# Optimization experiments

Measured on AMD Instinct MI355X. Metric: run time of the kernel, lower is better.

## Reference

```python
import jax, jax.numpy as jnp
import numpy as np
from jax.ops import segment_sum, segment_max

N = 50000
E = 800000
F_IN = 128
F_HEAD = 32
HEADS = 8
N_CLASSES = 32
NEG_SLOPE = 0.2


def setup_inputs() -> dict:
    key = jax.random.key(0)
    ks = jax.random.split(key, 12)
    x = jax.random.normal(ks[0], (N, F_IN), dtype=jnp.float32)
    edge_index = jax.random.randint(ks[1], (2, E), 0, N, dtype=jnp.int64)
    # layer 1 params (in=128 -> heads=8, out=32)
    s1 = 1.0 / np.sqrt(F_IN)
    W1 = jax.random.uniform(ks[2], (F_IN, HEADS * F_HEAD), jnp.float32, -s1, s1)
    a_src1 = jax.random.uniform(ks[3], (HEADS, F_HEAD), jnp.float32, -s1, s1)
    a_dst1 = jax.random.uniform(ks[4], (HEADS, F_HEAD), jnp.float32, -s1, s1)
    b1 = jnp.zeros((HEADS * F_HEAD,), jnp.float32)
    # layer 2 params (in=256 -> heads=1, out=32)
    s2 = 1.0 / np.sqrt(HEADS * F_HEAD)
    W2 = jax.random.uniform(ks[5], (HEADS * F_HEAD, N_CLASSES), jnp.float32, -s2, s2)
    a_src2 = jax.random.uniform(ks[6], (1, N_CLASSES), jnp.float32, -s2, s2)
    a_dst2 = jax.random.uniform(ks[7], (1, N_CLASSES), jnp.float32, -s2, s2)
    b2 = jnp.zeros((N_CLASSES,), jnp.float32)
    return {"x": x, "edge_index": edge_index, "W1": W1, "a_src1": a_src1,
            "a_dst1": a_dst1, "b1": b1, "W2": W2, "a_src2": a_src2,
            "a_dst2": a_dst2, "b2": b2}


def gat_conv(x, W, a_src, a_dst, b, src, dst, heads, out_ch):
    n = x.shape[0]
    h = (x @ W).reshape(n, heads, out_ch)                  # [N,H,F]
    alpha_src = jnp.einsum('nhf,hf->nh', h, a_src)         # [N,H]
    alpha_dst = jnp.einsum('nhf,hf->nh', h, a_dst)
    e = alpha_src[src] + alpha_dst[dst]                    # [E,H]
    e = jnp.where(e > 0, e, NEG_SLOPE * e)                 # LeakyReLU(0.2)
    # segment softmax over edges grouped by destination node
    m = segment_max(e, dst, num_segments=n)                # [N,H]
    ex = jnp.exp(e - m[dst])
    denom = segment_sum(ex, dst, num_segments=n)           # [N,H]
    alpha = ex / (denom[dst] + 1e-16)                      # [E,H]
    out = segment_sum(alpha[:, :, None] * h[src], dst, num_segments=n)  # [N,H,F]
    return out.reshape(n, heads * out_ch) + b


def reference(x, edge_index, W1, a_src1, a_dst1, b1, W2, a_src2, a_dst2, b2):
    src, dst = edge_index[0], edge_index[1]
    h = gat_conv(x, W1, a_src1, a_dst1, b1, src, dst, HEADS, F_HEAD)
    h = jax.nn.elu(h)
    out = gat_conv(h, W2, a_src2, a_dst2, b2, src, dst, 1, N_CLASSES)
    return out
```

## Files before the change

### kernel.cpp

```cpp
#include <hip/hip_runtime.h>
#include <math.h>

#define NNODES 50000
#define NEDGES 800000
#define GB 782

typedef _Float16 f16;
typedef _Float16 f16x8 __attribute__((ext_vector_type(8)));
typedef _Float16 f16x4 __attribute__((ext_vector_type(4)));
typedef _Float16 f16x2 __attribute__((ext_vector_type(2)));
typedef float f32x4 __attribute__((ext_vector_type(4)));
typedef float f32x8 __attribute__((ext_vector_type(8)));


__global__ __launch_bounds__(256) void k_deg_wfrag(const int* __restrict__ ei, int* __restrict__ deg,
                                                   int* __restrict__ rank,
                                                   const float* __restrict__ W1, const float* __restrict__ W2,
                                                   f16* __restrict__ W1f, f16* __restrict__ W2f) {
    int bid = blockIdx.x;
    if (bid < NEDGES / 256) {
        int e = bid * 256 + threadIdx.x;
        rank[e] = atomicAdd(&deg[ei[NEDGES + e]], 1);
    } else {
        int id = (bid - NEDGES / 256) * 256 + threadIdx.x;
        if (id < 32768) {
            int k = id >> 8, c = id & 255;
            int kc = k >> 5, quad = (k & 31) >> 3, j = k & 7;
            W1f[(((kc << 8) + c) * 4 + quad) * 8 + j] = (f16)W1[id];
        } else {
            int i2 = id - 32768;
            int k = i2 >> 5, c = i2 & 31;
            int kc = k >> 5, quad = (k & 31) >> 3, j = k & 7;
            W2f[(((kc << 5) + c) * 4 + quad) * 8 + j] = (f16)W2[i2];
        }
    }
}

__global__ __launch_bounds__(256) void k_scanA(const int* __restrict__ deg, int* __restrict__ incl,
                                               int* __restrict__ partial) {
    int t = threadIdx.x;
    int i = blockIdx.x * 256 + t;
    int v = (i < NNODES) ? deg[i] : 0;
    int lane = t & 63, wid = t >> 6;
    int s = v;
#pragma unroll
    for (int d = 1; d < 64; d <<= 1) { int u = __shfl_up(s, d, 64); if (lane >= d) s += u; }
    __shared__ int wtot[4];
    if (lane == 63) wtot[wid] = s;
    __syncthreads();
    int off = 0;
    for (int w = 0; w < wid; ++w) off += wtot[w];
    s += off;
    if (i < NNODES) incl[i] = s;
    if (t == 255) partial[blockIdx.x] = s;
}

__global__ __launch_bounds__(256) void k_scanC(const int* __restrict__ deg, const int* __restrict__ incl,
                                               const int* __restrict__ partial, int* __restrict__ rowst) {
    int t = threadIdx.x, bid = blockIdx.x;
    int v = (t < bid) ? partial[t] : 0;
    int lane = t & 63, wid = t >> 6;
#pragma unroll
    for (int d = 1; d < 64; d <<= 1) v += __shfl_xor(v, d);
    __shared__ int ws[4];
    if (lane == 0) ws[wid] = v;
    __syncthreads();
    int choff = ws[0] + ws[1] + ws[2] + ws[3];
    int i = bid * 256 + t;
    if (i < NNODES) {
        int rs1 = incl[i] + choff;
        rowst[i + 1] = rs1;
        if (i == 0) rowst[0] = 0;
    }
}


__global__ __launch_bounds__(256) void k_gemm1_sc(const float* __restrict__ X, const f16* __restrict__ W1f,
                                                  const float* __restrict__ Asrc, const float* __restrict__ Adst,
                                                  f16* __restrict__ h1h, float* __restrict__ as1,
                                                  float* __restrict__ ad1, const int* __restrict__ ei,
                                                  const int* __restrict__ rowst, const int* __restrict__ rank,
                                                  unsigned* __restrict__ sd_csr) {
    __shared__ f16 sA[64 * 136];
    int bid = blockIdx.x;
    int t = threadIdx.x;
    if (bid >= GB) {
        int e = (bid - GB) * 256 + t;
        if (e < NEDGES) {
            int s = ei[e], d = ei[NEDGES + e];
            int pos = rowst[d] + rank[e];
            sd_csr[pos] = ((unsigned)d << 16) | (unsigned)s;
        }
        return;
    }
    int bm = bid * 64;
#pragma unroll
    for (int i = 0; i < 8; ++i) {
        int idx = i * 256 + t;
        int row = idx >> 5, c4 = (idx & 31) << 2;
        int gr = bm + row;
        float4 v = make_float4(0.f, 0.f, 0.f, 0.f);
        if (gr < NNODES) v = *(const float4*)(X + (size_t)gr * 128 + c4);
        f16x4 h = {(f16)v.x, (f16)v.y, (f16)v.z, (f16)v.w};
        *(f16x4*)&sA[row * 136 + c4] = h;
    }
    __syncthreads();
    int lane = t & 63, w = t >> 6;
    int r = lane & 15, quad = lane >> 4;
    int r0 = w * 16;
    f32x4 acc[2][8];
#pragma unroll
    for (int h2 = 0; h2 < 2; ++h2)
#pragma unroll
        for (int nt = 0; nt < 8; ++nt) acc[h2][nt] = (f32x4){0.f, 0.f, 0.f, 0.f};
#pragma unroll
    for (int kc = 0; kc < 4; ++kc) {
        f16x8 a = *(f16x8*)&sA[(r0 + r) * 136 + kc * 32 + quad * 8];
#pragma unroll
        for (int h2 = 0; h2 < 2; ++h2)
#pragma unroll
            for (int nt = 0; nt < 8; ++nt) {
                f16x8 b = *(const f16x8*)&W1f[(((kc << 8) + h2 * 128 + nt * 16 + r) * 4 + quad) * 8];
                acc[h2][nt] = __builtin_amdgcn_mfma_f32_16x16x32_f16(a, b, acc[h2][nt], 0, 0, 0);
            }
    }
#pragma unroll
    for (int h2 = 0; h2 < 2; ++h2)
#pragma unroll
        for (int nt = 0; nt < 8; ++nt)
#pragma unroll
            for (int i = 0; i < 4; ++i) {
                int gr = bm + r0 + quad * 4 + i;
                if (gr < NNODES) h1h[(size_t)gr * 256 + h2 * 128 + nt * 16 + r] = (f16)acc[h2][nt][i];
            }
#pragma unroll
    for (int h2 = 0; h2 < 2; ++h2) {
        float asv[8], adv[8];
#pragma unroll
        for (int nt = 0; nt < 8; ++nt) {
            asv[nt] = Asrc[h2 * 128 + nt * 16 + r];
            adv[nt] = Adst[h2 * 128 + nt * 16 + r];
        }
#pragma unroll
        for (int i = 0; i < 4; ++i) {
            int gr = bm + r0 + quad * 4 + i;
#pragma unroll
            for (int hl = 0; hl < 4; ++hl) {
                float ps = acc[h2][2 * hl][i] * asv[2 * hl] + acc[h2][2 * hl + 1][i] * asv[2 * hl + 1];
                float pd = acc[h2][2 * hl][i] * adv[2 * hl] + acc[h2][2 * hl + 1][i] * adv[2 * hl + 1];
#pragma unroll
                for (int off = 1; off < 16; off <<= 1) {
                    ps += __shfl_xor(ps, off);
                    pd += __shfl_xor(pd, off);
                }
                if (r == 0 && gr < NNODES) {
                    as1[(size_t)gr * 8 + h2 * 4 + hl] = ps;
                    ad1[(size_t)gr * 8 + h2 * 4 + hl] = pd;
                }
            }
        }
    }
}

__global__ __launch_bounds__(256) void k_gemm2(const f16* __restrict__ h2h, const f16* __restrict__ W2f,
                                               const float* __restrict__ Asrc, const float* __restrict__ Adst,
                                               f16* __restrict__ gh, float* __restrict__ as2,
                                               float* __restrict__ ad2) {
    int t = threadIdx.x;
    int bm = blockIdx.x * 64;
    int lane = t & 63, w = t >> 6;
    int r = lane & 15, quad = lane >> 4;
    int r0 = w * 16;
    int gra = bm + r0 + r;
    int grac = gra < NNODES ? gra : 0;
    f32x4 acc[2];
    acc[0] = (f32x4){0.f, 0.f, 0.f, 0.f};
    acc[1] = (f32x4){0.f, 0.f, 0.f, 0.f};
#pragma unroll
    for (int kc = 0; kc < 8; ++kc) {
        f16x8 a = *(const f16x8*)(h2h + (size_t)grac * 256 + kc * 32 + quad * 8);
#pragma unroll
        for (int nt = 0; nt < 2; ++nt) {
            f16x8 b = *(const f16x8*)&W2f[(((kc << 5) + nt * 16 + r) * 4 + quad) * 8];
            acc[nt] = __builtin_amdgcn_mfma_f32_16x16x32_f16(a, b, acc[nt], 0, 0, 0);
        }
    }
#pragma unroll
    for (int nt = 0; nt < 2; ++nt)
#pragma unroll
        for (int i = 0; i < 4; ++i) {
            int gr = bm + r0 + quad * 4 + i;
            if (gr < NNODES) gh[(size_t)gr * 32 + nt * 16 + r] = (f16)acc[nt][i];
        }
    float as0 = Asrc[r], as16 = Asrc[16 + r];
    float ad0 = Adst[r], ad16 = Adst[16 + r];
#pragma unroll
    for (int i = 0; i < 4; ++i) {
        int gr = bm + r0 + quad * 4 + i;
        float ps = acc[0][i] * as0 + acc[1][i] * as16;
        float pd = acc[0][i] * ad0 + acc[1][i] * ad16;
#pragma unroll
        for (int off = 1; off < 16; off <<= 1) {
            ps += __shfl_xor(ps, off);
            pd += __shfl_xor(pd, off);
        }
        if (r == 0 && gr < NNODES) { as2[gr] = ps; ad2[gr] = pd; }
    }
}


__global__ __launch_bounds__(256) void k_agg1(const int* __restrict__ rowst, const unsigned* __restrict__ sd_csr,
                                              const float* __restrict__ as1, const float* __restrict__ ad1,
                                              const f16* __restrict__ h1h, const float* __restrict__ b1,
                                              f16* __restrict__ h2h) {
    int w = threadIdx.x >> 6, lane = threadIdx.x & 63;
    int n = blockIdx.x * 4 + w;
    int s = rowst[n], e = rowst[n + 1];
    int slot = lane >> 5;
    int ch32 = lane & 31;
    int c0 = ch32 << 3;
    int hm = ch32 >> 2;
    float adn = ad1[(size_t)n * 8 + hm];
    const f16* __restrict__ hp = h1h + c0;
    const float* __restrict__ ap = as1 + hm;
    f32x8 acc = (f32x8){0.f, 0.f, 0.f, 0.f, 0.f, 0.f, 0.f, 0.f};
    float sum = 0.f;
    int j = s + slot;
    for (; j + 14 < e; j += 16) {
        int si[8];
#pragma unroll
        for (int u = 0; u < 8; ++u) si[u] = (int)(sd_csr[j + 2 * u] & 0xffffu);
        float xv[8];
#pragma unroll
        for (int u = 0; u < 8; ++u) xv[u] = ap[(size_t)si[u] * 8];
        f16x8 vv[8];
#pragma unroll
        for (int u = 0; u < 8; ++u) vv[u] = *(const f16x8*)(hp + (size_t)si[u] * 256);
#pragma unroll
        for (int u = 0; u < 8; ++u) {
            float x = xv[u] + adn;
            x = fmaxf(x, 0.2f * x);
            float ee = __expf(x);
            sum += ee;
#pragma unroll
            for (int k = 0; k < 8; ++k) acc[k] += ee * (float)vv[u][k];
        }
    }
    for (; j + 6 < e; j += 8) {
        int si[4];
#pragma unroll
        for (int u = 0; u < 4; ++u) si[u] = (int)(sd_csr[j + 2 * u] & 0xffffu);
        float xv[4];
#pragma unroll
        for (int u = 0; u < 4; ++u) xv[u] = ap[(size_t)si[u] * 8];
        f16x8 vv[4];
#pragma unroll
        for (int u = 0; u < 4; ++u) vv[u] = *(const f16x8*)(hp + (size_t)si[u] * 256);
#pragma unroll
        for (int u = 0; u < 4; ++u) {
            float x = xv[u] + adn;
            x = fmaxf(x, 0.2f * x);
            float ee = __expf(x);
            sum += ee;
#pragma unroll
            for (int k = 0; k < 8; ++k) acc[k] += ee * (float)vv[u][k];
        }
    }
    for (; j < e; j += 2) {
        int s0 = (int)(sd_csr[j] & 0xffffu);
        float x0 = ap[(size_t)s0 * 8] + adn;
        f16x8 v0 = *(const f16x8*)(hp + (size_t)s0 * 256);
        x0 = fmaxf(x0, 0.2f * x0);
        float e0 = __expf(x0);
        sum += e0;
#pragma unroll
        for (int k = 0; k < 8; ++k) acc[k] += e0 * (float)v0[k];
    }
    sum += __shfl_xor(sum, 32);
#pragma unroll
    for (int k = 0; k < 8; ++k) acc[k] += __shfl_xor(acc[k], 32);
    if (slot == 0) {
        float inv = 1.f / (sum + 1e-16f);
        float4 b0 = *(const float4*)(b1 + c0);
        float4 b4 = *(const float4*)(b1 + c0 + 4);
        float o[8] = {acc[0] * inv + b0.x, acc[1] * inv + b0.y, acc[2] * inv + b0.z, acc[3] * inv + b0.w,
                      acc[4] * inv + b4.x, acc[5] * inv + b4.y, acc[6] * inv + b4.z, acc[7] * inv + b4.w};
        f16x8 oh;
#pragma unroll
        for (int k = 0; k < 8; ++k) {
            float v = o[k];
            v = v > 0.f ? v : __expf(v) - 1.f;
            oh[k] = (f16)v;
        }
        *(f16x8*)(h2h + (size_t)n * 256 + c0) = oh;
    }
}

__global__ __launch_bounds__(256) void k_agg2(const int* __restrict__ rowst, const unsigned* __restrict__ sd_csr,
                                              const float* __restrict__ as2, const float* __restrict__ ad2,
                                              const f16* __restrict__ gh, const float* __restrict__ b2,
                                              float* __restrict__ out) {
    int w = threadIdx.x >> 6, lane = threadIdx.x & 63;
    int n = blockIdx.x * 4 + w;
    int s = rowst[n], e = rowst[n + 1];
    int slot = lane >> 4;
    int cp = lane & 15;
    float adn = ad2[n];
    const f16* __restrict__ gp = gh + 2 * cp;
    float a0 = 0.f, a1 = 0.f, sum = 0.f;
    int j = s + slot;
    for (; j + 12 < e; j += 16) {
        int si[4];
#pragma unroll
        for (int u = 0; u < 4; ++u) si[u] = (int)(sd_csr[j + 4 * u] & 0xffffu);
        float xv[4];
#pragma unroll
        for (int u = 0; u < 4; ++u) xv[u] = as2[si[u]];
        f16x2 vv[4];
#pragma unroll
        for (int u = 0; u < 4; ++u) vv[u] = *(const f16x2*)(gp + (size_t)si[u] * 32);
#pragma unroll
        for (int u = 0; u < 4; ++u) {
            float x = xv[u] + adn;
            x = fmaxf(x, 0.2f * x);
            float ee = __expf(x);
            sum += ee;
            a0 += ee * (float)vv[u][0];
            a1 += ee * (float)vv[u][1];
        }
    }
    for (; j + 4 < e; j += 8) {
        int s0 = (int)(sd_csr[j] & 0xffffu);
        int s1 = (int)(sd_csr[j + 4] & 0xffffu);
        float x0 = as2[s0] + adn, x1 = as2[s1] + adn;
        f16x2 v0 = *(const f16x2*)(gp + (size_t)s0 * 32);
        f16x2 v1 = *(const f16x2*)(gp + (size_t)s1 * 32);
        x0 = fmaxf(x0, 0.2f * x0);
        x1 = fmaxf(x1, 0.2f * x1);
        float e0 = __expf(x0), e1 = __expf(x1);
        sum += e0 + e1;
        a0 += e0 * (float)v0[0] + e1 * (float)v1[0];
        a1 += e0 * (float)v0[1] + e1 * (float)v1[1];
    }
    for (; j < e; j += 4) {
        int s0 = (int)(sd_csr[j] & 0xffffu);
        float x0 = as2[s0] + adn;
        f16x2 v0 = *(const f16x2*)(gp + (size_t)s0 * 32);
        x0 = fmaxf(x0, 0.2f * x0);
        float e0 = __expf(x0);
        sum += e0;
        a0 += e0 * (float)v0[0];
        a1 += e0 * (float)v0[1];
    }
#pragma unroll
    for (int d = 16; d < 64; d <<= 1) {
        sum += __shfl_xor(sum, d);
        a0 += __shfl_xor(a0, d);
        a1 += __shfl_xor(a1, d);
    }
    if (slot == 0) {
        float inv = 1.f / (sum + 1e-16f);
        float2 o;
        o.x = a0 * inv + b2[2 * cp];
        o.y = a1 * inv + b2[2 * cp + 1];
        *(float2*)(out + (size_t)n * 32 + 2 * cp) = o;
    }
}


extern "C" void kernel_launch(void* const* d_in, const int* in_sizes, int n_in,
                              void* d_out, int out_size, void* d_ws, size_t ws_size,
                              hipStream_t stream) {
    const float* x    = (const float*)d_in[0];
    const int*   ei   = (const int*)d_in[1];
    const float* W1   = (const float*)d_in[2];
    const float* As1  = (const float*)d_in[3];
    const float* Ad1  = (const float*)d_in[4];
    const float* b1   = (const float*)d_in[5];
    const float* W2   = (const float*)d_in[6];
    const float* As2  = (const float*)d_in[7];
    const float* Ad2  = (const float*)d_in[8];
    const float* b2   = (const float*)d_in[9];
    float* out = (float*)d_out;

    char* p = (char*)d_ws;
    auto alloc = [&](size_t bytes) -> char* {
        char* r = p;
        p += (bytes + 255) & ~(size_t)255;
        return r;
    };
    f16* h1h      = (f16*)alloc((size_t)NNODES * 256 * 2);
    f16* h2h      = (f16*)alloc((size_t)NNODES * 256 * 2);
    f16* W1f      = (f16*)alloc((size_t)128 * 256 * 2);
    f16* W2f      = (f16*)alloc((size_t)256 * 32 * 2);
    f16* gh       = (f16*)alloc((size_t)NNODES * 32 * 2);
    float* asrc1  = (float*)alloc((size_t)NNODES * 8 * 4);
    float* adst1  = (float*)alloc((size_t)NNODES * 8 * 4);
    float* asrc2  = (float*)alloc((size_t)NNODES * 4);
    float* adst2  = (float*)alloc((size_t)NNODES * 4);
    int* deg      = (int*)alloc((size_t)NNODES * 4);
    int* incl     = (int*)alloc((size_t)NNODES * 4);
    int* rowst    = (int*)alloc((size_t)(NNODES + 1) * 4);
    int* rank     = (int*)alloc((size_t)NEDGES * 4);
    unsigned* sdc = (unsigned*)alloc((size_t)NEDGES * 4);
    int* partial  = (int*)alloc(256 * 4);

    const int EB = NEDGES / 256;
    const int NCH = (NNODES + 255) / 256;

    hipMemsetAsync(deg, 0, (size_t)NNODES * 4, stream);
    k_deg_wfrag<<<EB + 160, 256, 0, stream>>>(ei, deg, rank, W1, W2, W1f, W2f);
    k_scanA<<<NCH, 256, 0, stream>>>(deg, incl, partial);
    k_scanC<<<NCH, 256, 0, stream>>>(deg, incl, partial, rowst);

    k_gemm1_sc<<<GB + EB, 256, 0, stream>>>(x, W1f, As1, Ad1, h1h, asrc1, adst1, ei, rowst, rank, sdc);
    k_agg1<<<NNODES / 4, 256, 0, stream>>>(rowst, sdc, asrc1, adst1, h1h, b1, h2h);

    k_gemm2<<<(NNODES + 63) / 64, 256, 0, stream>>>(h2h, W2f, As2, Ad2, gh, asrc2, adst2);
    k_agg2<<<NNODES / 4, 256, 0, stream>>>(rowst, sdc, asrc2, adst2, gh, b2, out);
}
```

Measured before the change: 265.8 us.

## Store CSR sources as u16 and keep W1 fragments in registers per column slice

```diff
diff --git a/kernel.cpp b/kernel.cpp
--- a/kernel.cpp
+++ b/kernel.cpp
@@ -11,6 +11,7 @@
 typedef _Float16 f16x2 __attribute__((ext_vector_type(2)));
 typedef float f32x4 __attribute__((ext_vector_type(4)));
 typedef float f32x8 __attribute__((ext_vector_type(8)));
+typedef unsigned short u16;
 
 
 __global__ __launch_bounds__(256) void k_deg_wfrag(const int* __restrict__ ei, int* __restrict__ deg,
@@ -80,7 +81,7 @@
                                                   f16* __restrict__ h1h, float* __restrict__ as1,
                                                   float* __restrict__ ad1, const int* __restrict__ ei,
                                                   const int* __restrict__ rowst, const int* __restrict__ rank,
-                                                  unsigned* __restrict__ sd_csr) {
+                                                  u16* __restrict__ sd16) {
     __shared__ f16 sA[64 * 136];
     int bid = blockIdx.x;
     int t = threadIdx.x;
@@ -89,11 +90,20 @@
         if (e < NEDGES) {
             int s = ei[e], d = ei[NEDGES + e];
             int pos = rowst[d] + rank[e];
-            sd_csr[pos] = ((unsigned)d << 16) | (unsigned)s;
+            sd16[pos] = (u16)s;
         }
         return;
     }
     int bm = bid * 64;
+    int lane = t & 63, w = t >> 6;
+    int r = lane & 15, quad = lane >> 4;
+    int cw = w * 64;
+    f16x8 bf[4][4];
+#pragma unroll
+    for (int kc = 0; kc < 4; ++kc)
+#pragma unroll
+        for (int nt = 0; nt < 4; ++nt)
+            bf[kc][nt] = *(const f16x8*)&W1f[(((kc << 8) + cw + nt * 16 + r) * 4 + quad) * 8];
 #pragma unroll
     for (int i = 0; i < 8; ++i) {
         int idx = i * 256 + t;
@@ -105,61 +115,55 @@
         *(f16x4*)&sA[row * 136 + c4] = h;
     }
     __syncthreads();
-    int lane = t & 63, w = t >> 6;
-    int r = lane & 15, quad = lane >> 4;
-    int r0 = w * 16;
-    f32x4 acc[2][8];
-#pragma unroll
-    for (int h2 = 0; h2 < 2; ++h2)
-#pragma unroll
-        for (int nt = 0; nt < 8; ++nt) acc[h2][nt] = (f32x4){0.f, 0.f, 0.f, 0.f};
-#pragma unroll
-    for (int kc = 0; kc < 4; ++kc) {
-        f16x8 a = *(f16x8*)&sA[(r0 + r) * 136 + kc * 32 + quad * 8];
-#pragma unroll
-        for (int h2 = 0; h2 < 2; ++h2)
-#pragma unroll
-            for (int nt = 0; nt < 8; ++nt) {
-                f16x8 b = *(const f16x8*)&W1f[(((kc << 8) + h2 * 128 + nt * 16 + r) * 4 + quad) * 8];
-                acc[h2][nt] = __builtin_amdgcn_mfma_f32_16x16x32_f16(a, b, acc[h2][nt], 0, 0, 0);
+    f32x4 acc[4][4];
+#pragma unroll
+    for (int rg = 0; rg < 4; ++rg)
+#pragma unroll
+        for (int nt = 0; nt < 4; ++nt) acc[rg][nt] = (f32x4){0.f, 0.f, 0.f, 0.f};
+#pragma unroll
+    for (int kc = 0; kc < 4; ++kc)
+#pragma unroll
+        for (int rg = 0; rg < 4; ++rg) {
+            f16x8 a = *(f16x8*)&sA[(rg * 16 + r) * 136 + kc * 32 + quad * 8];
+#pragma unroll
+            for (int nt = 0; nt < 4; ++nt)
+                acc[rg][nt] = __builtin_amdgcn_mfma_f32_16x16x32_f16(a, bf[kc][nt], acc[rg][nt], 0, 0, 0);
+        }
+#pragma unroll
+    for (int rg = 0; rg < 4; ++rg)
+#pragma unroll
+        for (int nt = 0; nt < 4; ++nt)
+#pragma unroll
+            for (int i = 0; i < 4; ++i) {
+                int gr = bm + rg * 16 + quad * 4 + i;
+                if (gr < NNODES) h1h[(size_t)gr * 256 + cw + nt * 16 + r] = (f16)acc[rg][nt][i];
             }
-    }
-#pragma unroll
-    for (int h2 = 0; h2 < 2; ++h2)
-#pragma unroll
-        for (int nt = 0; nt < 8; ++nt)
-#pragma unroll
-            for (int i = 0; i < 4; ++i) {
-                int gr = bm + r0 + quad * 4 + i;
-                if (gr < NNODES) h1h[(size_t)gr * 256 + h2 * 128 + nt * 16 + r] = (f16)acc[h2][nt][i];
-            }
-#pragma unroll
-    for (int h2 = 0; h2 < 2; ++h2) {
-        float asv[8], adv[8];
-#pragma unroll
-        for (int nt = 0; nt < 8; ++nt) {
-            asv[nt] = Asrc[h2 * 128 + nt * 16 + r];
-            adv[nt] = Adst[h2 * 128 + nt * 16 + r];
-        }
+    float asv[4], adv[4];
+#pragma unroll
+    for (int nt = 0; nt < 4; ++nt) {
+        asv[nt] = Asrc[cw + nt * 16 + r];
+        adv[nt] = Adst[cw + nt * 16 + r];
+    }
+#pragma unroll
+    for (int rg = 0; rg < 4; ++rg)
 #pragma unroll
         for (int i = 0; i < 4; ++i) {
-            int gr = bm + r0 + quad * 4 + i;
-#pragma unroll
-            for (int hl = 0; hl < 4; ++hl) {
-                float ps = acc[h2][2 * hl][i] * asv[2 * hl] + acc[h2][2 * hl + 1][i] * asv[2 * hl + 1];
-                float pd = acc[h2][2 * hl][i] * adv[2 * hl] + acc[h2][2 * hl + 1][i] * adv[2 * hl + 1];
+            int gr = bm + rg * 16 + quad * 4 + i;
+#pragma unroll
+            for (int hh = 0; hh < 2; ++hh) {
+                float ps = acc[rg][2 * hh][i] * asv[2 * hh] + acc[rg][2 * hh + 1][i] * asv[2 * hh + 1];
+                float pd = acc[rg][2 * hh][i] * adv[2 * hh] + acc[rg][2 * hh + 1][i] * adv[2 * hh + 1];
 #pragma unroll
                 for (int off = 1; off < 16; off <<= 1) {
                     ps += __shfl_xor(ps, off);
                     pd += __shfl_xor(pd, off);
                 }
                 if (r == 0 && gr < NNODES) {
-                    as1[(size_t)gr * 8 + h2 * 4 + hl] = ps;
-                    ad1[(size_t)gr * 8 + h2 * 4 + hl] = pd;
+                    as1[(size_t)gr * 8 + 2 * w + hh] = ps;
+                    ad1[(size_t)gr * 8 + 2 * w + hh] = pd;
                 }
             }
         }
-    }
 }
 
 __global__ __launch_bounds__(256) void k_gemm2(const f16* __restrict__ h2h, const f16* __restrict__ W2f,
@@ -209,7 +213,7 @@
 }
 
 
-__global__ __launch_bounds__(256) void k_agg1(const int* __restrict__ rowst, const unsigned* __restrict__ sd_csr,
+__global__ __launch_bounds__(256) void k_agg1(const int* __restrict__ rowst, const u16* __restrict__ sd16,
                                               const float* __restrict__ as1, const float* __restrict__ ad1,
                                               const f16* __restrict__ h1h, const float* __restrict__ b1,
                                               f16* __restrict__ h2h) {
@@ -229,7 +233,7 @@
     for (; j + 14 < e; j += 16) {
         int si[8];
 #pragma unroll
-        for (int u = 0; u < 8; ++u) si[u] = (int)(sd_csr[j + 2 * u] & 0xffffu);
+        for (int u = 0; u < 8; ++u) si[u] = (int)sd16[j + 2 * u];
         float xv[8];
 #pragma unroll
         for (int u = 0; u < 8; ++u) xv[u] = ap[(size_t)si[u] * 8];
@@ -249,7 +253,7 @@
     for (; j + 6 < e; j += 8) {
         int si[4];
 #pragma unroll
-        for (int u = 0; u < 4; ++u) si[u] = (int)(sd_csr[j + 2 * u] & 0xffffu);
+        for (int u = 0; u < 4; ++u) si[u] = (int)sd16[j + 2 * u];
         float xv[4];
 #pragma unroll
         for (int u = 0; u < 4; ++u) xv[u] = ap[(size_t)si[u] * 8];
@@ -267,7 +271,7 @@
         }
     }
     for (; j < e; j += 2) {
-        int s0 = (int)(sd_csr[j] & 0xffffu);
+        int s0 = (int)sd16[j];
         float x0 = ap[(size_t)s0 * 8] + adn;
         f16x8 v0 = *(const f16x8*)(hp + (size_t)s0 * 256);
         x0 = fmaxf(x0, 0.2f * x0);
@@ -296,7 +300,7 @@
     }
 }
 
-__global__ __launch_bounds__(256) void k_agg2(const int* __restrict__ rowst, const unsigned* __restrict__ sd_csr,
+__global__ __launch_bounds__(256) void k_agg2(const int* __restrict__ rowst, const u16* __restrict__ sd16,
                                               const float* __restrict__ as2, const float* __restrict__ ad2,
                                               const f16* __restrict__ gh, const float* __restrict__ b2,
                                               float* __restrict__ out) {
@@ -312,7 +316,7 @@
     for (; j + 12 < e; j += 16) {
         int si[4];
 #pragma unroll
-        for (int u = 0; u < 4; ++u) si[u] = (int)(sd_csr[j + 4 * u] & 0xffffu);
+        for (int u = 0; u < 4; ++u) si[u] = (int)sd16[j + 4 * u];
         float xv[4];
 #pragma unroll
         for (int u = 0; u < 4; ++u) xv[u] = as2[si[u]];
@@ -330,8 +334,8 @@
         }
     }
     for (; j + 4 < e; j += 8) {
-        int s0 = (int)(sd_csr[j] & 0xffffu);
-        int s1 = (int)(sd_csr[j + 4] & 0xffffu);
+        int s0 = (int)sd16[j];
+        int s1 = (int)sd16[j + 4];
         float x0 = as2[s0] + adn, x1 = as2[s1] + adn;
         f16x2 v0 = *(const f16x2*)(gp + (size_t)s0 * 32);
         f16x2 v1 = *(const f16x2*)(gp + (size_t)s1 * 32);
@@ -343,7 +347,7 @@
         a1 += e0 * (float)v0[1] + e1 * (float)v1[1];
     }
     for (; j < e; j += 4) {
-        int s0 = (int)(sd_csr[j] & 0xffffu);
+        int s0 = (int)sd16[j];
         float x0 = as2[s0] + adn;
         f16x2 v0 = *(const f16x2*)(gp + (size_t)s0 * 32);
         x0 = fmaxf(x0, 0.2f * x0);
@@ -402,7 +406,7 @@
     int* incl     = (int*)alloc((size_t)NNODES * 4);
     int* rowst    = (int*)alloc((size_t)(NNODES + 1) * 4);
     int* rank     = (int*)alloc((size_t)NEDGES * 4);
-    unsigned* sdc = (unsigned*)alloc((size_t)NEDGES * 4);
+    u16* sdc      = (u16*)alloc((size_t)NEDGES * 2);
     int* partial  = (int*)alloc(256 * 4);
 
     const int EB = NEDGES / 256;
```

Result: faster. 254.2 us (-4.4%).
